# Kernel optimization log

Measured on AMD Instinct MI355X. Metric: run time of the kernel, lower is better.

## Reference

```python
import jax, jax.numpy as jnp
import numpy as np


def setup_inputs() -> dict:
    key = jax.random.key(0)
    k1, k2, k3, k4 = jax.random.split(key, 4)
    B, T, IN, D = 32, 256, 64, 128
    x = jax.random.normal(k1, (B, T, IN), dtype=jnp.float32)
    h0 = jnp.zeros((B, D), dtype=jnp.float32)
    Wx = jax.random.normal(k2, (IN, D), dtype=jnp.float32) * 0.01
    Wgate = jax.random.normal(k3, (D, D), dtype=jnp.float32) * 0.01
    Wh = jax.random.normal(k4, (D, D), dtype=jnp.float32) * 0.01
    return {"x": x, "h0": h0, "Wx": Wx, "Wgate": Wgate, "Wh": Wh}


def reference(x, h0, Wx, Wgate, Wh):
    # x: (B, T, in_dim); h0: (B, dim); returns (h_final, y, hidden_grads, dh_dWh)
    def step_single(h_r, x_r):
        # per-sample gated update: h_r (dim,), x_r (in_dim,)
        pre = x_r @ Wx + h_r @ Wh
        a = jax.nn.gelu(pre, approximate=False)  # torch GELU() is the exact erf variant
        g = jax.nn.sigmoid(a @ Wgate)
        hn = g * h_r + (1.0 - g)
        return hn, hn

    # per-step, per-sample Jacobian d h_new / d h  (mirrors vmap(jacrev(..., argnums=1)))
    jac_batched = jax.vmap(jax.jacrev(step_single, argnums=0, has_aux=True))

    def body(h, x_t):  # h: (B, dim), x_t: (B, in_dim)
        jac, h_new = jac_batched(h, x_t)  # jac: (B, dim, dim)
        return h_new, (h_new, jac)

    xt = jnp.swapaxes(x, 0, 1)  # (T, B, in_dim)
    h_final, (ys, jacs) = jax.lax.scan(body, h0, xt)
    y = jnp.swapaxes(ys, 0, 1)  # (B, T, dim)

    # last-step Jacobian wrt Wh, evaluated with the post-update h (as in the torch code)
    x_last = x[:, -1, :]

    def f_wh(Wh_):
        pre = x_last @ Wx + h_final @ Wh_
        a = jax.nn.gelu(pre, approximate=False)
        g = jax.nn.sigmoid(a @ Wgate)
        return g * h_final + (1.0 - g)

    dh_dWh = jax.jacrev(f_wh)(Wh)  # (B, dim, dim, dim)
    return (h_final, y, jacs, dh_dWh)
```

## Files before the change

### kernel.cpp

```cpp
#include <hip/hip_runtime.h>


#define JACOFF 1052672L
#define DHWOFF 135270400L

typedef __attribute__((ext_vector_type(8))) short frag_ab;
typedef __attribute__((ext_vector_type(4))) float frag_cd;

__device__ __forceinline__ short f2bf(float f) {
    unsigned u = __builtin_bit_cast(unsigned, f);
    unsigned r = (u + 0x7fffu + ((u >> 16) & 1u)) >> 16;
    return (short)r;
}

__device__ __forceinline__ void wg_barrier() {
    asm volatile("s_waitcnt lgkmcnt(0)\n\ts_barrier" ::: "memory");
}

__device__ __forceinline__ float dpp_xor1(float x) {
    int r = __builtin_amdgcn_mov_dpp(__builtin_bit_cast(int, x), 0xB1, 0xF, 0xF, true);
    return __builtin_bit_cast(float, r);
}
__device__ __forceinline__ float dpp_xor2(float x) {
    int r = __builtin_amdgcn_mov_dpp(__builtin_bit_cast(int, x), 0x4E, 0xF, 0xF, true);
    return __builtin_bit_cast(float, r);
}

__global__ __launch_bounds__(256) void prep_xw_kernel(
    const float* __restrict__ Wh, const float* __restrict__ Wg,
    const float* __restrict__ x, const float* __restrict__ Wx,
    float* __restrict__ whT, float* __restrict__ wgT, float* __restrict__ xw)
{
    int blk = blockIdx.x;
    int tid = threadIdx.x;
    if (blk < 128) {
        int idx = blk * 256 + tid;
        if (idx < 16384) {
            int k = idx >> 7, i = idx & 127;
            whT[i * 128 + k] = Wh[idx];
        } else {
            int r = idx - 16384;
            int k = r >> 7, i = r & 127;
            wgT[i * 128 + k] = Wg[r];
        }
        return;
    }
    __shared__ float xs[2][64];
    int sub = tid >> 7;
    int bt = (blk - 128) * 2 + sub;
    int i = tid & 127;
    if (i < 64) xs[sub][i] = x[bt * 64 + i];
    __syncthreads();
    float acc = 0.f;
#pragma unroll
    for (int m = 0; m < 64; ++m)
        acc += xs[sub][m] * Wx[m * 128 + i];
    xw[bt * 128 + i] = acc;
}

__global__ __launch_bounds__(512, 1) void scan_pk_kernel(
    const float* __restrict__ xw, const float* __restrict__ h0,
    const float* __restrict__ whT, const float* __restrict__ wgT,
    const float* __restrict__ Wgate, const float* __restrict__ Wh,
    float* __restrict__ out,
    short* __restrict__ Abf, float* __restrict__ wgv, float* __restrict__ wc,
    float* __restrict__ wdF, float* __restrict__ wuF, float* __restrict__ whF,
    short* __restrict__ PT)
{
    int tid = threadIdx.x;
    if (blockIdx.x >= 32) {
        int c = (blockIdx.x - 32) * 32 + (tid >> 4);
        int k0 = (tid & 15) * 8;
        int i = c >> 7, j = c & 127;
        short v[8];
#pragma unroll
        for (int m = 0; m < 8; ++m) {
            float wg = Wgate[(k0 + m) * 128 + i];
            float wh = Wh[j * 128 + k0 + m];
            v[m] = f2bf(wg * wh);
        }
        *(frag_ab*)(PT + (long)c * 128 + k0) = *(frag_ab*)v;
        return;
    }

    const int b = blockIdx.x;
    const int i = tid >> 2, qtr = tid & 3;
    __shared__ float hbuf[2][128];
    __shared__ float abuf[128];
    float wh[32], wgc[32];
    {
        const float* whr = whT + i * 128 + qtr * 32;
        const float* wgr = wgT + i * 128 + qtr * 32;
#pragma unroll
        for (int k = 0; k < 32; k += 4) {
            float4 a4 = *(const float4*)(whr + k);
            wh[k] = a4.x; wh[k + 1] = a4.y; wh[k + 2] = a4.z; wh[k + 3] = a4.w;
            float4 b4 = *(const float4*)(wgr + k);
            wgc[k] = b4.x; wgc[k + 1] = b4.y; wgc[k + 2] = b4.z; wgc[k + 3] = b4.w;
        }
    }
    if (qtr == 0) hbuf[0][i] = h0[b * 128 + i];
    __syncthreads();

    const float inv_sqrt2 = 0.70710678118654752f;
    const float inv_sqrt2pi = 0.39894228040143268f;

    float xwv = xw[(b * 256 + 0) * 128 + i];
    float xw1 = xw[(b * 256 + 1) * 128 + i];

    for (int t = 0; t < 256; ++t) {
        int p = t & 1;
        int tn = (t < 254) ? t + 2 : 255;
        float xw2 = xw[(b * 256 + tn) * 128 + i];

        float s0 = 0.f, s1 = 0.f, s2 = 0.f, s3 = 0.f;
        const float* hb = &hbuf[p][qtr * 32];
#pragma unroll
        for (int k = 0; k < 32; k += 4) {
            float4 h4 = *(const float4*)(hb + k);
            s0 += h4.x * wh[k];
            s1 += h4.y * wh[k + 1];
            s2 += h4.z * wh[k + 2];
            s3 += h4.w * wh[k + 3];
        }
        float s = (s0 + s1) + (s2 + s3);
        s += dpp_xor1(s);
        s += dpp_xor2(s);
        float pre = xwv + s;

        float cdf = 0.5f * (1.0f + erff(pre * inv_sqrt2));
        float a = pre * cdf;
        float dval = cdf + pre * inv_sqrt2pi * expf(-0.5f * pre * pre);

        long tb = (long)(t * 32 + b) * 128 + i;
        if (qtr == 0) {
            Abf[tb] = f2bf(dval);
            abuf[i] = a;
        }
        wg_barrier();

        float r0 = 0.f, r1 = 0.f, r2 = 0.f, r3 = 0.f;
        const float* ab = &abuf[qtr * 32];
#pragma unroll
        for (int k = 0; k < 32; k += 4) {
            float4 a4 = *(const float4*)(ab + k);
            r0 += a4.x * wgc[k];
            r1 += a4.y * wgc[k + 1];
            r2 += a4.z * wgc[k + 2];
            r3 += a4.w * wgc[k + 3];
        }
        float r = (r0 + r1) + (r2 + r3);
        r += dpp_xor1(r);
        r += dpp_xor2(r);
        float g = 1.0f / (1.0f + expf(-r));
        float hp = hbuf[p][i];
        float c = (hp - 1.0f) * g * (1.0f - g);
        float hn = g * hp + 1.0f - g;
        if (qtr == 0) {
            hbuf[p ^ 1][i] = hn;
            wgv[tb] = g;
            wc[tb] = c;
            out[4096 + (b * 256 + t) * 128 + i] = hn;
        }
        xwv = xw1; xw1 = xw2;
        wg_barrier();
    }

    float hfin = hbuf[0][i];
    if (qtr == 0) {
        out[b * 128 + i] = hfin;
        whF[b * 128 + i] = hfin;
    }

    {
        float s0 = 0.f, s1 = 0.f, s2 = 0.f, s3 = 0.f;
        const float* hb = &hbuf[0][qtr * 32];
#pragma unroll
        for (int k = 0; k < 32; k += 4) {
            float4 h4 = *(const float4*)(hb + k);
            s0 += h4.x * wh[k];
            s1 += h4.y * wh[k + 1];
            s2 += h4.z * wh[k + 2];
            s3 += h4.w * wh[k + 3];
        }
        float s = (s0 + s1) + (s2 + s3);
        s += dpp_xor1(s);
        s += dpp_xor2(s);
        float pre = xwv + s;
        float cdf = 0.5f * (1.0f + erff(pre * inv_sqrt2));
        float a = pre * cdf;
        float dval = cdf + pre * inv_sqrt2pi * expf(-0.5f * pre * pre);
        if (qtr == 0) {
            wdF[b * 128 + i] = dval;
            abuf[i] = a;
        }
        __syncthreads();
        float r0 = 0.f, r1 = 0.f, r2 = 0.f, r3 = 0.f;
        const float* ab = &abuf[qtr * 32];
#pragma unroll
        for (int k = 0; k < 32; k += 4) {
            float4 a4 = *(const float4*)(ab + k);
            r0 += a4.x * wgc[k];
            r1 += a4.y * wgc[k + 1];
            r2 += a4.z * wgc[k + 2];
            r3 += a4.w * wgc[k + 3];
        }
        float r = (r0 + r1) + (r2 + r3);
        r += dpp_xor1(r);
        r += dpp_xor2(r);
        float g = 1.0f / (1.0f + expf(-r));
        if (qtr == 0) wuF[b * 128 + i] = (hfin - 1.0f) * g * (1.0f - g);
    }
}

__global__ __launch_bounds__(256) void jacmm_dhdw_kernel(
    const short* __restrict__ Abf,
    const short* __restrict__ PT,
    const float* __restrict__ wgv,
    const float* __restrict__ wc,
    const float* __restrict__ Wgate,
    const float* __restrict__ dF, const float* __restrict__ uF, const float* __restrict__ hF,
    float* __restrict__ out)
{
    int bx = blockIdx.x;
    int tid = threadIdx.x;
    int grp = bx / 3, rem = bx % 3;

    if (rem == 2) {
        __shared__ float hs[128], dsh[128];
        int b = grp >> 7, i = grp & 127;
        if (tid < 128) {
            hs[tid] = hF[b * 128 + tid];
            dsh[tid] = dF[b * 128 + tid];
        }
        __syncthreads();
        float u = uF[b * 128 + i];
        int q0 = (tid & 31) * 4, p0 = (tid >> 5) * 16;
        float w0 = u * dsh[q0 + 0] * Wgate[(q0 + 0) * 128 + i];
        float w1 = u * dsh[q0 + 1] * Wgate[(q0 + 1) * 128 + i];
        float w2 = u * dsh[q0 + 2] * Wgate[(q0 + 2) * 128 + i];
        float w3 = u * dsh[q0 + 3] * Wgate[(q0 + 3) * 128 + i];
        float* dst = out + DHWOFF + (long)grp * 16384;
#pragma unroll
        for (int pp = 0; pp < 16; ++pp) {
            float hp = hs[p0 + pp];
            *(float4*)(dst + (p0 + pp) * 128 + q0) = make_float4(hp * w0, hp * w1, hp * w2, hp * w3);
        }
        return;
    }

    int jb = grp * 2 + rem;
    int rb = jb & 63;
    int cb = jb >> 6;

    const short* Ag = Abf + (long)rb * (128 * 128);
    const short* Bg = PT + (long)cb * (128 * 128);

    int w = tid >> 6;
    int lane = tid & 63;
    int wr = w >> 1;
    int wcol = w & 1;
    int lrow = lane & 15;
    int quad = lane >> 4;

    long rowbase = (long)rb * 128;
    float ci[4][4], gi[4][4];
#pragma unroll
    for (int p = 0; p < 4; ++p) {
        int trow0 = wr * 64 + p * 16 + quad * 4;
#pragma unroll
        for (int reg = 0; reg < 4; ++reg) {
            long row = rowbase + trow0 + reg;
            ci[p][reg] = wc[row * 128 + cb];
            gi[p][reg] = wgv[row * 128 + cb];
        }
    }

    frag_cd acc[4][4];
#pragma unroll
    for (int p = 0; p < 4; ++p)
#pragma unroll
        for (int q = 0; q < 4; ++q) {
            acc[p][q][0] = 0.f; acc[p][q][1] = 0.f; acc[p][q][2] = 0.f; acc[p][q][3] = 0.f;
        }

#pragma unroll
    for (int kk = 0; kk < 4; ++kk) {
        int ko8 = (kk * 4 + quad) * 8;
        frag_ab af[4], bf[4];
#pragma unroll
        for (int p = 0; p < 4; ++p) {
            int r = wr * 64 + p * 16 + lrow;
            af[p] = *(const frag_ab*)(Ag + r * 128 + ko8);
        }
#pragma unroll
        for (int q = 0; q < 4; ++q) {
            int n = wcol * 64 + q * 16 + lrow;
            bf[q] = *(const frag_ab*)(Bg + n * 128 + ko8);
        }
#pragma unroll
        for (int p = 0; p < 4; ++p)
#pragma unroll
            for (int q = 0; q < 4; ++q)
                acc[p][q] = __builtin_amdgcn_mfma_f32_16x16x32_bf16(af[p], bf[q], acc[p][q], 0, 0, 0);
    }

#pragma unroll
    for (int p = 0; p < 4; ++p) {
        int trow0 = wr * 64 + p * 16 + quad * 4;
#pragma unroll
        for (int reg = 0; reg < 4; ++reg) {
            long row = rowbase + trow0 + reg;
            float* orow = out + JACOFF + row * 16384 + (long)cb * 128;
#pragma unroll
            for (int q = 0; q < 4; ++q) {
                int tcol = wcol * 64 + q * 16 + lrow;
                float v = ci[p][reg] * acc[p][q][reg];
                if (tcol == cb) v += gi[p][reg];
                orow[tcol] = v;
            }
        }
    }
}

extern "C" void kernel_launch(void* const* d_in, const int* in_sizes, int n_in,
                              void* d_out, int out_size, void* d_ws, size_t ws_size,
                              hipStream_t stream)
{
    (void)in_sizes; (void)n_in; (void)out_size; (void)ws_size;
    const float* x     = (const float*)d_in[0];
    const float* h0    = (const float*)d_in[1];
    const float* Wx    = (const float*)d_in[2];
    const float* Wgate = (const float*)d_in[3];
    const float* Wh    = (const float*)d_in[4];
    float* out = (float*)d_out;
    float* ws  = (float*)d_ws;

    float* xw  = ws;
    float* whT = ws + 1048576;
    float* wgT = ws + 1064960;
    float* wgv = ws + 1081344;
    float* wc  = ws + 2129920;
    float* wdF = ws + 3178496;
    float* wuF = ws + 3182592;
    float* whF = ws + 3186688;
    short* Abf = (short*)(ws + 3190784);
    short* PT  = (short*)(ws + 3715072);

    prep_xw_kernel<<<4224, 256, 0, stream>>>(Wh, Wgate, x, Wx, whT, wgT, xw);
    scan_pk_kernel<<<544, 512, 0, stream>>>(xw, h0, whT, wgT, Wgate, Wh, out,
                                            Abf, wgv, wc, wdF, wuF, whF, PT);
    jacmm_dhdw_kernel<<<12288, 256, 0, stream>>>(Abf, PT, wgv, wc, Wgate, wdF, wuF, whF, out);
}
```

Measured before the change: 1.130 ms.

## Fuse scan and Jacobian GEMM into persistent kernel with flag-based overlap

Merges the sequential scan and the Jacobian/dWh output kernels into one persistent kernel. 32 blocks run the recurrence and publish per-16-step progress counters, while the remaining blocks pull work tiles from an atomic counter and start each Jacobian GEMM tile as soon as its timesteps are ready. The PT precompute moves into the prep kernel. The aim is to hide the long serial scan behind the bandwidth-heavy Jacobian writes, at the cost of spin-waiting and relying on all 256 blocks being co-resident.

```diff
diff --git a/kernel.cpp b/kernel.cpp
--- a/kernel.cpp
+++ b/kernel.cpp
@@ -3,6 +3,9 @@
 
 #define JACOFF 1052672L
 #define DHWOFF 135270400L
+
+#define NTICK_JAC   8192u
+#define NTICK_TOTAL 10240u
 
 typedef __attribute__((ext_vector_type(8))) short frag_ab;
 typedef __attribute__((ext_vector_type(4))) float frag_cd;
@@ -26,10 +29,11 @@
     return __builtin_bit_cast(float, r);
 }
 
-__global__ __launch_bounds__(256) void prep_xw_kernel(
+__global__ __launch_bounds__(256) void prep_kernel(
     const float* __restrict__ Wh, const float* __restrict__ Wg,
     const float* __restrict__ x, const float* __restrict__ Wx,
-    float* __restrict__ whT, float* __restrict__ wgT, float* __restrict__ xw)
+    float* __restrict__ whT, float* __restrict__ wgT, float* __restrict__ xw,
+    short* __restrict__ PT, unsigned* __restrict__ ctrl)
 {
     int blk = blockIdx.x;
     int tid = threadIdx.x;
@@ -45,281 +49,309 @@
         }
         return;
     }
-    __shared__ float xs[2][64];
-    int sub = tid >> 7;
-    int bt = (blk - 128) * 2 + sub;
-    int i = tid & 127;
-    if (i < 64) xs[sub][i] = x[bt * 64 + i];
-    __syncthreads();
-    float acc = 0.f;
-#pragma unroll
-    for (int m = 0; m < 64; ++m)
-        acc += xs[sub][m] * Wx[m * 128 + i];
-    xw[bt * 128 + i] = acc;
-}
-
-__global__ __launch_bounds__(512, 1) void scan_pk_kernel(
+    if (blk < 4224) {
+        __shared__ float xs[2][64];
+        int sub = tid >> 7;
+        int bt = (blk - 128) * 2 + sub;
+        int i = tid & 127;
+        if (i < 64) xs[sub][i] = x[bt * 64 + i];
+        __syncthreads();
+        float acc = 0.f;
+#pragma unroll
+        for (int m = 0; m < 64; ++m)
+            acc += xs[sub][m] * Wx[m * 128 + i];
+        xw[bt * 128 + i] = acc;
+        return;
+    }
+    if (blk < 5248) {
+        int c = (blk - 4224) * 16 + (tid >> 4);
+        int k0 = (tid & 15) * 8;
+        int i = c >> 7, j = c & 127;
+        short v[8];
+#pragma unroll
+        for (int m = 0; m < 8; ++m) {
+            float wg = Wg[(k0 + m) * 128 + i];
+            float wh = Wh[j * 128 + k0 + m];
+            v[m] = f2bf(wg * wh);
+        }
+        *(frag_ab*)(PT + (long)c * 128 + k0) = *(frag_ab*)v;
+        return;
+    }
+    if (tid < 128) ctrl[tid] = 0u;
+}
+
+__global__ __launch_bounds__(512, 2) void fused_kernel(
     const float* __restrict__ xw, const float* __restrict__ h0,
     const float* __restrict__ whT, const float* __restrict__ wgT,
-    const float* __restrict__ Wgate, const float* __restrict__ Wh,
+    const float* __restrict__ Wgate,
     float* __restrict__ out,
     short* __restrict__ Abf, float* __restrict__ wgv, float* __restrict__ wc,
     float* __restrict__ wdF, float* __restrict__ wuF, float* __restrict__ whF,
-    short* __restrict__ PT)
+    const short* __restrict__ PT, unsigned* __restrict__ ctrl)
 {
-    int tid = threadIdx.x;
-    if (blockIdx.x >= 32) {
-        int c = (blockIdx.x - 32) * 32 + (tid >> 4);
-        int k0 = (tid & 15) * 8;
-        int i = c >> 7, j = c & 127;
-        short v[8];
-#pragma unroll
-        for (int m = 0; m < 8; ++m) {
-            float wg = Wgate[(k0 + m) * 128 + i];
-            float wh = Wh[j * 128 + k0 + m];
-            v[m] = f2bf(wg * wh);
-        }
-        *(frag_ab*)(PT + (long)c * 128 + k0) = *(frag_ab*)v;
-        return;
-    }
-
-    const int b = blockIdx.x;
-    const int i = tid >> 2, qtr = tid & 3;
+    const int tid = threadIdx.x;
     __shared__ float hbuf[2][128];
     __shared__ float abuf[128];
-    float wh[32], wgc[32];
-    {
-        const float* whr = whT + i * 128 + qtr * 32;
-        const float* wgr = wgT + i * 128 + qtr * 32;
-#pragma unroll
-        for (int k = 0; k < 32; k += 4) {
-            float4 a4 = *(const float4*)(whr + k);
-            wh[k] = a4.x; wh[k + 1] = a4.y; wh[k + 2] = a4.z; wh[k + 3] = a4.w;
-            float4 b4 = *(const float4*)(wgr + k);
-            wgc[k] = b4.x; wgc[k + 1] = b4.y; wgc[k + 2] = b4.z; wgc[k + 3] = b4.w;
-        }
-    }
-    if (qtr == 0) hbuf[0][i] = h0[b * 128 + i];
-    __syncthreads();
-
-    const float inv_sqrt2 = 0.70710678118654752f;
-    const float inv_sqrt2pi = 0.39894228040143268f;
-
-    float xwv = xw[(b * 256 + 0) * 128 + i];
-    float xw1 = xw[(b * 256 + 1) * 128 + i];
-
-    for (int t = 0; t < 256; ++t) {
-        int p = t & 1;
-        int tn = (t < 254) ? t + 2 : 255;
-        float xw2 = xw[(b * 256 + tn) * 128 + i];
-
-        float s0 = 0.f, s1 = 0.f, s2 = 0.f, s3 = 0.f;
-        const float* hb = &hbuf[p][qtr * 32];
-#pragma unroll
-        for (int k = 0; k < 32; k += 4) {
-            float4 h4 = *(const float4*)(hb + k);
-            s0 += h4.x * wh[k];
-            s1 += h4.y * wh[k + 1];
-            s2 += h4.z * wh[k + 2];
-            s3 += h4.w * wh[k + 3];
-        }
-        float s = (s0 + s1) + (s2 + s3);
-        s += dpp_xor1(s);
-        s += dpp_xor2(s);
-        float pre = xwv + s;
-
-        float cdf = 0.5f * (1.0f + erff(pre * inv_sqrt2));
-        float a = pre * cdf;
-        float dval = cdf + pre * inv_sqrt2pi * expf(-0.5f * pre * pre);
-
-        long tb = (long)(t * 32 + b) * 128 + i;
+    __shared__ float hs2[2][128];
+    __shared__ float ds2[2][128];
+    __shared__ unsigned sh_u;
+
+    if (blockIdx.x < 32) {
+        const int b = blockIdx.x;
+        const int i = tid >> 2, qtr = tid & 3;
+        float wh[32], wgc[32];
+        {
+            const float* whr = whT + i * 128 + qtr * 32;
+            const float* wgr = wgT + i * 128 + qtr * 32;
+#pragma unroll
+            for (int k = 0; k < 32; k += 4) {
+                float4 a4 = *(const float4*)(whr + k);
+                wh[k] = a4.x; wh[k + 1] = a4.y; wh[k + 2] = a4.z; wh[k + 3] = a4.w;
+                float4 b4 = *(const float4*)(wgr + k);
+                wgc[k] = b4.x; wgc[k + 1] = b4.y; wgc[k + 2] = b4.z; wgc[k + 3] = b4.w;
+            }
+        }
+        if (qtr == 0) hbuf[0][i] = h0[b * 128 + i];
+        __syncthreads();
+
+        const float inv_sqrt2 = 0.70710678118654752f;
+        const float inv_sqrt2pi = 0.39894228040143268f;
+
+        float xwv = xw[(b * 256 + 0) * 128 + i];
+        float xw1 = xw[(b * 256 + 1) * 128 + i];
+
+        for (int t = 0; t < 256; ++t) {
+            int p = t & 1;
+            int tn = (t < 254) ? t + 2 : 255;
+            float xw2 = xw[(b * 256 + tn) * 128 + i];
+
+            float s0 = 0.f, s1 = 0.f, s2 = 0.f, s3 = 0.f;
+            const float* hb = &hbuf[p][qtr * 32];
+#pragma unroll
+            for (int k = 0; k < 32; k += 4) {
+                float4 h4 = *(const float4*)(hb + k);
+                s0 += h4.x * wh[k];
+                s1 += h4.y * wh[k + 1];
+                s2 += h4.z * wh[k + 2];
+                s3 += h4.w * wh[k + 3];
+            }
+            float s = (s0 + s1) + (s2 + s3);
+            s += dpp_xor1(s);
+            s += dpp_xor2(s);
+            float pre = xwv + s;
+
+            float cdf = 0.5f * (1.0f + erff(pre * inv_sqrt2));
+            float a = pre * cdf;
+            float dval = cdf + pre * inv_sqrt2pi * expf(-0.5f * pre * pre);
+
+            long tb = (long)(t * 32 + b) * 128 + i;
+            if (qtr == 0) {
+                __hip_atomic_store(&Abf[tb], f2bf(dval), __ATOMIC_RELAXED, __HIP_MEMORY_SCOPE_AGENT);
+                abuf[i] = a;
+            }
+            wg_barrier();
+
+            float r0 = 0.f, r1 = 0.f, r2 = 0.f, r3 = 0.f;
+            const float* ab = &abuf[qtr * 32];
+#pragma unroll
+            for (int k = 0; k < 32; k += 4) {
+                float4 a4 = *(const float4*)(ab + k);
+                r0 += a4.x * wgc[k];
+                r1 += a4.y * wgc[k + 1];
+                r2 += a4.z * wgc[k + 2];
+                r3 += a4.w * wgc[k + 3];
+            }
+            float r = (r0 + r1) + (r2 + r3);
+            r += dpp_xor1(r);
+            r += dpp_xor2(r);
+            float g = 1.0f / (1.0f + expf(-r));
+            float hp = hbuf[p][i];
+            float c = (hp - 1.0f) * g * (1.0f - g);
+            float hn = g * hp + 1.0f - g;
+            if (qtr == 0) {
+                hbuf[p ^ 1][i] = hn;
+                __hip_atomic_store(&wgv[tb], g, __ATOMIC_RELAXED, __HIP_MEMORY_SCOPE_AGENT);
+                __hip_atomic_store(&wc[tb], c, __ATOMIC_RELAXED, __HIP_MEMORY_SCOPE_AGENT);
+                out[4096 + (b * 256 + t) * 128 + i] = hn;
+            }
+            xwv = xw1; xw1 = xw2;
+            wg_barrier();
+
+            if ((t & 15) == 15) {
+                __syncthreads();
+                if (tid == 0)
+                    __hip_atomic_fetch_add(&ctrl[t >> 4], 1u, __ATOMIC_RELAXED, __HIP_MEMORY_SCOPE_AGENT);
+            }
+        }
+
+        float hfin = hbuf[0][i];
         if (qtr == 0) {
-            Abf[tb] = f2bf(dval);
-            abuf[i] = a;
-        }
-        wg_barrier();
-
-        float r0 = 0.f, r1 = 0.f, r2 = 0.f, r3 = 0.f;
-        const float* ab = &abuf[qtr * 32];
-#pragma unroll
-        for (int k = 0; k < 32; k += 4) {
-            float4 a4 = *(const float4*)(ab + k);
-            r0 += a4.x * wgc[k];
-            r1 += a4.y * wgc[k + 1];
-            r2 += a4.z * wgc[k + 2];
-            r3 += a4.w * wgc[k + 3];
-        }
-        float r = (r0 + r1) + (r2 + r3);
-        r += dpp_xor1(r);
-        r += dpp_xor2(r);
-        float g = 1.0f / (1.0f + expf(-r));
-        float hp = hbuf[p][i];
-        float c = (hp - 1.0f) * g * (1.0f - g);
-        float hn = g * hp + 1.0f - g;
-        if (qtr == 0) {
-            hbuf[p ^ 1][i] = hn;
-            wgv[tb] = g;
-            wc[tb] = c;
-            out[4096 + (b * 256 + t) * 128 + i] = hn;
-        }
-        xwv = xw1; xw1 = xw2;
-        wg_barrier();
-    }
-
-    float hfin = hbuf[0][i];
-    if (qtr == 0) {
-        out[b * 128 + i] = hfin;
-        whF[b * 128 + i] = hfin;
-    }
-
-    {
-        float s0 = 0.f, s1 = 0.f, s2 = 0.f, s3 = 0.f;
-        const float* hb = &hbuf[0][qtr * 32];
-#pragma unroll
-        for (int k = 0; k < 32; k += 4) {
-            float4 h4 = *(const float4*)(hb + k);
-            s0 += h4.x * wh[k];
-            s1 += h4.y * wh[k + 1];
-            s2 += h4.z * wh[k + 2];
-            s3 += h4.w * wh[k + 3];
-        }
-        float s = (s0 + s1) + (s2 + s3);
-        s += dpp_xor1(s);
-        s += dpp_xor2(s);
-        float pre = xwv + s;
-        float cdf = 0.5f * (1.0f + erff(pre * inv_sqrt2));
-        float a = pre * cdf;
-        float dval = cdf + pre * inv_sqrt2pi * expf(-0.5f * pre * pre);
-        if (qtr == 0) {
-            wdF[b * 128 + i] = dval;
-            abuf[i] = a;
-        }
-        __syncthreads();
-        float r0 = 0.f, r1 = 0.f, r2 = 0.f, r3 = 0.f;
-        const float* ab = &abuf[qtr * 32];
-#pragma unroll
-        for (int k = 0; k < 32; k += 4) {
-            float4 a4 = *(const float4*)(ab + k);
-            r0 += a4.x * wgc[k];
-            r1 += a4.y * wgc[k + 1];
-            r2 += a4.z * wgc[k + 2];
-            r3 += a4.w * wgc[k + 3];
-        }
-        float r = (r0 + r1) + (r2 + r3);
-        r += dpp_xor1(r);
-        r += dpp_xor2(r);
-        float g = 1.0f / (1.0f + expf(-r));
-        if (qtr == 0) wuF[b * 128 + i] = (hfin - 1.0f) * g * (1.0f - g);
-    }
-}
-
-__global__ __launch_bounds__(256) void jacmm_dhdw_kernel(
-    const short* __restrict__ Abf,
-    const short* __restrict__ PT,
-    const float* __restrict__ wgv,
-    const float* __restrict__ wc,
-    const float* __restrict__ Wgate,
-    const float* __restrict__ dF, const float* __restrict__ uF, const float* __restrict__ hF,
-    float* __restrict__ out)
-{
-    int bx = blockIdx.x;
-    int tid = threadIdx.x;
-    int grp = bx / 3, rem = bx % 3;
-
-    if (rem == 2) {
-        __shared__ float hs[128], dsh[128];
-        int b = grp >> 7, i = grp & 127;
-        if (tid < 128) {
-            hs[tid] = hF[b * 128 + tid];
-            dsh[tid] = dF[b * 128 + tid];
-        }
-        __syncthreads();
-        float u = uF[b * 128 + i];
-        int q0 = (tid & 31) * 4, p0 = (tid >> 5) * 16;
-        float w0 = u * dsh[q0 + 0] * Wgate[(q0 + 0) * 128 + i];
-        float w1 = u * dsh[q0 + 1] * Wgate[(q0 + 1) * 128 + i];
-        float w2 = u * dsh[q0 + 2] * Wgate[(q0 + 2) * 128 + i];
-        float w3 = u * dsh[q0 + 3] * Wgate[(q0 + 3) * 128 + i];
-        float* dst = out + DHWOFF + (long)grp * 16384;
-#pragma unroll
-        for (int pp = 0; pp < 16; ++pp) {
-            float hp = hs[p0 + pp];
-            *(float4*)(dst + (p0 + pp) * 128 + q0) = make_float4(hp * w0, hp * w1, hp * w2, hp * w3);
-        }
-        return;
-    }
-
-    int jb = grp * 2 + rem;
-    int rb = jb & 63;
-    int cb = jb >> 6;
-
-    const short* Ag = Abf + (long)rb * (128 * 128);
-    const short* Bg = PT + (long)cb * (128 * 128);
-
-    int w = tid >> 6;
-    int lane = tid & 63;
-    int wr = w >> 1;
-    int wcol = w & 1;
-    int lrow = lane & 15;
-    int quad = lane >> 4;
-
-    long rowbase = (long)rb * 128;
-    float ci[4][4], gi[4][4];
-#pragma unroll
-    for (int p = 0; p < 4; ++p) {
-        int trow0 = wr * 64 + p * 16 + quad * 4;
-#pragma unroll
-        for (int reg = 0; reg < 4; ++reg) {
-            long row = rowbase + trow0 + reg;
-            ci[p][reg] = wc[row * 128 + cb];
-            gi[p][reg] = wgv[row * 128 + cb];
-        }
-    }
-
-    frag_cd acc[4][4];
-#pragma unroll
-    for (int p = 0; p < 4; ++p)
-#pragma unroll
-        for (int q = 0; q < 4; ++q) {
-            acc[p][q][0] = 0.f; acc[p][q][1] = 0.f; acc[p][q][2] = 0.f; acc[p][q][3] = 0.f;
-        }
-
-#pragma unroll
-    for (int kk = 0; kk < 4; ++kk) {
-        int ko8 = (kk * 4 + quad) * 8;
-        frag_ab af[4], bf[4];
-#pragma unroll
-        for (int p = 0; p < 4; ++p) {
-            int r = wr * 64 + p * 16 + lrow;
-            af[p] = *(const frag_ab*)(Ag + r * 128 + ko8);
-        }
-#pragma unroll
-        for (int q = 0; q < 4; ++q) {
-            int n = wcol * 64 + q * 16 + lrow;
-            bf[q] = *(const frag_ab*)(Bg + n * 128 + ko8);
-        }
-#pragma unroll
-        for (int p = 0; p < 4; ++p)
-#pragma unroll
-            for (int q = 0; q < 4; ++q)
-                acc[p][q] = __builtin_amdgcn_mfma_f32_16x16x32_bf16(af[p], bf[q], acc[p][q], 0, 0, 0);
-    }
-
-#pragma unroll
-    for (int p = 0; p < 4; ++p) {
-        int trow0 = wr * 64 + p * 16 + quad * 4;
-#pragma unroll
-        for (int reg = 0; reg < 4; ++reg) {
-            long row = rowbase + trow0 + reg;
-            float* orow = out + JACOFF + row * 16384 + (long)cb * 128;
-#pragma unroll
-            for (int q = 0; q < 4; ++q) {
-                int tcol = wcol * 64 + q * 16 + lrow;
-                float v = ci[p][reg] * acc[p][q][reg];
-                if (tcol == cb) v += gi[p][reg];
-                orow[tcol] = v;
-            }
-        }
+            out[b * 128 + i] = hfin;
+            __hip_atomic_store(&whF[b * 128 + i], hfin, __ATOMIC_RELAXED, __HIP_MEMORY_SCOPE_AGENT);
+        }
+
+        {
+            float s0 = 0.f, s1 = 0.f, s2 = 0.f, s3 = 0.f;
+            const float* hb = &hbuf[0][qtr * 32];
+#pragma unroll
+            for (int k = 0; k < 32; k += 4) {
+                float4 h4 = *(const float4*)(hb + k);
+                s0 += h4.x * wh[k];
+                s1 += h4.y * wh[k + 1];
+                s2 += h4.z * wh[k + 2];
+                s3 += h4.w * wh[k + 3];
+            }
+            float s = (s0 + s1) + (s2 + s3);
+            s += dpp_xor1(s);
+            s += dpp_xor2(s);
+            float pre = xwv + s;
+            float cdf = 0.5f * (1.0f + erff(pre * inv_sqrt2));
+            float a = pre * cdf;
+            float dval = cdf + pre * inv_sqrt2pi * expf(-0.5f * pre * pre);
+            if (qtr == 0) {
+                __hip_atomic_store(&wdF[b * 128 + i], dval, __ATOMIC_RELAXED, __HIP_MEMORY_SCOPE_AGENT);
+                abuf[i] = a;
+            }
+            __syncthreads();
+            float r0 = 0.f, r1 = 0.f, r2 = 0.f, r3 = 0.f;
+            const float* ab = &abuf[qtr * 32];
+#pragma unroll
+            for (int k = 0; k < 32; k += 4) {
+                float4 a4 = *(const float4*)(ab + k);
+                r0 += a4.x * wgc[k];
+                r1 += a4.y * wgc[k + 1];
+                r2 += a4.z * wgc[k + 2];
+                r3 += a4.w * wgc[k + 3];
+            }
+            float r = (r0 + r1) + (r2 + r3);
+            r += dpp_xor1(r);
+            r += dpp_xor2(r);
+            float g = 1.0f / (1.0f + expf(-r));
+            if (qtr == 0)
+                __hip_atomic_store(&wuF[b * 128 + i], (hfin - 1.0f) * g * (1.0f - g),
+                                   __ATOMIC_RELAXED, __HIP_MEMORY_SCOPE_AGENT);
+        }
+        __syncthreads();
+        if (tid == 0)
+            __hip_atomic_fetch_add(&ctrl[16], 1u, __ATOMIC_RELAXED, __HIP_MEMORY_SCOPE_AGENT);
+    }
+
+    const int lane = tid & 63;
+    for (;;) {
+        if (tid == 0)
+            sh_u = __hip_atomic_fetch_add(&ctrl[64], 1u, __ATOMIC_RELAXED, __HIP_MEMORY_SCOPE_AGENT);
+        __syncthreads();
+        unsigned u = sh_u;
+        if (u >= NTICK_TOTAL) break;
+
+        if (u < NTICK_JAC) {
+            int rb = (int)(u >> 7), cb = (int)(u & 127u);
+            int fidx = (4 * rb + 3) >> 4;
+            if (tid == 0) {
+                while (__hip_atomic_load(&ctrl[fidx], __ATOMIC_RELAXED, __HIP_MEMORY_SCOPE_AGENT) < 32u)
+                    __builtin_amdgcn_s_sleep(8);
+            }
+            __syncthreads();
+            __builtin_amdgcn_fence(__ATOMIC_ACQUIRE, "agent");
+
+            const short* Ag = Abf + (long)rb * (128 * 128);
+            const short* Bg = PT + (long)cb * (128 * 128);
+
+            int w = tid >> 6;
+            int wr = w >> 2;
+            int wcol = w & 3;
+            int lrow = lane & 15;
+            int quad = lane >> 4;
+
+            long rowbase = (long)rb * 128;
+            float ci[4][4], gi[4][4];
+#pragma unroll
+            for (int p = 0; p < 4; ++p) {
+                int trow0 = wr * 64 + p * 16 + quad * 4;
+#pragma unroll
+                for (int reg = 0; reg < 4; ++reg) {
+                    long row = rowbase + trow0 + reg;
+                    ci[p][reg] = wc[row * 128 + cb];
+                    gi[p][reg] = wgv[row * 128 + cb];
+                }
+            }
+
+            frag_cd acc[4][2];
+#pragma unroll
+            for (int p = 0; p < 4; ++p)
+#pragma unroll
+                for (int q = 0; q < 2; ++q) {
+                    acc[p][q][0] = 0.f; acc[p][q][1] = 0.f; acc[p][q][2] = 0.f; acc[p][q][3] = 0.f;
+                }
+
+#pragma unroll
+            for (int kk = 0; kk < 4; ++kk) {
+                int ko8 = (kk * 4 + quad) * 8;
+                frag_ab af[4], bf2[2];
+#pragma unroll
+                for (int p = 0; p < 4; ++p) {
+                    int r = wr * 64 + p * 16 + lrow;
+                    af[p] = *(const frag_ab*)(Ag + r * 128 + ko8);
+                }
+#pragma unroll
+                for (int q = 0; q < 2; ++q) {
+                    int n = wcol * 32 + q * 16 + lrow;
+                    bf2[q] = *(const frag_ab*)(Bg + n * 128 + ko8);
+                }
+#pragma unroll
+                for (int p = 0; p < 4; ++p)
+#pragma unroll
+                    for (int q = 0; q < 2; ++q)
+                        acc[p][q] = __builtin_amdgcn_mfma_f32_16x16x32_bf16(af[p], bf2[q], acc[p][q], 0, 0, 0);
+            }
+
+#pragma unroll
+            for (int p = 0; p < 4; ++p) {
+                int trow0 = wr * 64 + p * 16 + quad * 4;
+#pragma unroll
+                for (int reg = 0; reg < 4; ++reg) {
+                    long row = rowbase + trow0 + reg;
+                    float* orow = out + JACOFF + row * 16384 + (long)cb * 128;
+#pragma unroll
+                    for (int q = 0; q < 2; ++q) {
+                        int tcol = wcol * 32 + q * 16 + lrow;
+                        float v = ci[p][reg] * acc[p][q][reg];
+                        if (tcol == cb) v += gi[p][reg];
+                        orow[tcol] = v;
+                    }
+                }
+            }
+        } else {
+            if (tid == 0) {
+                while (__hip_atomic_load(&ctrl[16], __ATOMIC_RELAXED, __HIP_MEMORY_SCOPE_AGENT) < 32u)
+                    __builtin_amdgcn_s_sleep(8);
+            }
+            __syncthreads();
+            __builtin_amdgcn_fence(__ATOMIC_ACQUIRE, "agent");
+
+            int v = (int)(u - NTICK_JAC);
+            int half = tid >> 8, t2 = tid & 255;
+            int gu = v * 2 + half;
+            int b = gu >> 7, ii = gu & 127;
+            if (t2 < 128) {
+                hs2[half][t2] = whF[b * 128 + t2];
+                ds2[half][t2] = wdF[b * 128 + t2];
+            }
+            __syncthreads();
+            float u_ = wuF[b * 128 + ii];
+            int q0 = (t2 & 31) * 4, p0 = (t2 >> 5) * 16;
+            float w0 = u_ * ds2[half][q0 + 0] * Wgate[(q0 + 0) * 128 + ii];
+            float w1 = u_ * ds2[half][q0 + 1] * Wgate[(q0 + 1) * 128 + ii];
+            float w2 = u_ * ds2[half][q0 + 2] * Wgate[(q0 + 2) * 128 + ii];
+            float w3 = u_ * ds2[half][q0 + 3] * Wgate[(q0 + 3) * 128 + ii];
+            float* dst = out + DHWOFF + (long)gu * 16384;
+#pragma unroll
+            for (int pp = 0; pp < 16; ++pp) {
+                float hp = hs2[half][p0 + pp];
+                *(float4*)(dst + (p0 + pp) * 128 + q0) = make_float4(hp * w0, hp * w1, hp * w2, hp * w3);
+            }
+        }
+        __syncthreads();
     }
 }
 
@@ -346,9 +378,9 @@
     float* whF = ws + 3186688;
     short* Abf = (short*)(ws + 3190784);
     short* PT  = (short*)(ws + 3715072);
-
-    prep_xw_kernel<<<4224, 256, 0, stream>>>(Wh, Wgate, x, Wx, whT, wgT, xw);
-    scan_pk_kernel<<<544, 512, 0, stream>>>(xw, h0, whT, wgT, Wgate, Wh, out,
-                                            Abf, wgv, wc, wdF, wuF, whF, PT);
-    jacmm_dhdw_kernel<<<12288, 256, 0, stream>>>(Abf, PT, wgv, wc, Wgate, wdF, wuF, whF, out);
-}
+    unsigned* ctrl = (unsigned*)(ws + 4763648);
+
+    prep_kernel<<<5249, 256, 0, stream>>>(Wh, Wgate, x, Wx, whT, wgT, xw, PT, ctrl);
+    fused_kernel<<<256, 512, 0, stream>>>(xw, h0, whT, wgT, Wgate, out,
+                                          Abf, wgv, wc, wdF, wuF, whF, PT, ctrl);
+}
```

After: 1.373 ms. 21.6% more time.
